# Kernel tuning notes

Measured on AMD Instinct MI355X. Metric: run time of the kernel, lower is better.

The kernel has to match this reference:

```python
import jax, jax.numpy as jnp
import numpy as np

B, N, IN_DIM, D = 32, 2000, 3, 5
GROUP = 5
TOPK = 110

def setup_inputs() -> dict:
    key = jax.random.key(0)
    ks = jax.random.split(key, 11)
    def lin(k, fan_in, fan_out):
        kw, kb = jax.random.split(k)
        bound = 1.0 / np.sqrt(fan_in)
        W = jax.random.uniform(kw, (fan_in, fan_out), jnp.float32, -bound, bound)
        b = jax.random.uniform(kb, (fan_out,), jnp.float32, -bound, bound)
        return W, b
    Wi, bi = lin(ks[1], IN_DIM, D)
    Wq, bq = lin(ks[2], D, D)
    Wk, bk = lin(ks[3], D, D)
    Wv, bv = lin(ks[4], D, D)
    Wo, bo = lin(ks[5], D, D)
    in_mat = jax.random.normal(ks[0], (B, N, IN_DIM), jnp.float32)
    return {"in_mat": in_mat, "Wi": Wi, "bi": bi, "Wq": Wq, "bq": bq,
            "Wk": Wk, "bk": bk, "Wv": Wv, "bv": bv, "Wo": Wo, "bo": bo}

def reference(in_mat, Wi, bi, Wq, bq, Wk, bk, Wv, bv, Wo, bo):
    # input projection: [B,N,3] -> [B,N,D]
    x = in_mat @ Wi + bi
    Q = x @ Wq + bq
    K = x @ Wk + bk
    V = x @ Wv + bv
    scores = jnp.einsum('bnd,bmd->bnm', Q, K) / jnp.sqrt(jnp.float32(D))  # [B,N,N]
    attn = jax.nn.softmax(scores, axis=-1)
    context = jnp.einsum('bnm,bmd->bnd', attn, V)
    _out = context @ Wo + bo  # transformed output (unused downstream, as in source)

    # select_points, fully batched
    diag = jnp.diagonal(attn, axis1=1, axis2=2)               # [B,N]
    attn_sums = diag.reshape(B, N // GROUP, GROUP).sum(-1)    # [B, N/5]
    max_group_idx = jnp.argmax(attn_sums, axis=1)             # [B]
    grp_idx = max_group_idx[:, None] * GROUP + jnp.arange(GROUP)[None, :]  # [B,5]
    group_points = jnp.take_along_axis(in_mat, grp_idx[:, :, None], axis=1)  # [B,5,3]
    centroid = group_points.mean(axis=1)                       # [B,3]
    distances = jnp.linalg.norm(in_mat - centroid[:, None, :], axis=-1)  # [B,N]
    _, closest = jax.lax.top_k(-distances, TOPK)               # smallest distances, [B,110]
    selected = jnp.take_along_axis(in_mat, closest[:, :, None], axis=1)  # [B,110,3]
    return selected
```

## Files before the change

kernel.cpp:

```cpp
#include <hip/hip_runtime.h>
#include <stdint.h>

#define BB     32
#define NN     2000
#define TOPK_  110
#define NBIN   2048

__global__ __launch_bounds__(1024) void k_diag(
    const float* __restrict__ in_mat,
    const float* __restrict__ Wi, const float* __restrict__ bi,
    const float* __restrict__ Wq, const float* __restrict__ bq,
    const float* __restrict__ Wk, const float* __restrict__ bk,
    float* __restrict__ diag_out)
{
    __shared__ float4 Ps[2048];
    __shared__ float  partial[16][256];

    const int b     = blockIdx.y;
    const int chunk = blockIdx.x;
    const int t     = threadIdx.x;
    const float* inb = in_mat + (size_t)b * NN * 3;

    const float pf = 0.44721359549995793f * 1.4426950408889634f;
    float Mq[15], Mk[15], cq[5];
#pragma unroll
    for (int d = 0; d < 5; ++d) {
        float s = bq[d];
#pragma unroll
        for (int k = 0; k < 5; ++k) s += bi[k] * Wq[k * 5 + d];
        cq[d] = s;
    }
#pragma unroll
    for (int i = 0; i < 3; ++i)
#pragma unroll
        for (int d = 0; d < 5; ++d) {
            float sq = 0.f, sk = 0.f;
#pragma unroll
            for (int k = 0; k < 5; ++k) {
                sq += Wi[i * 5 + k] * Wq[k * 5 + d];
                sk += Wi[i * 5 + k] * Wk[k * 5 + d];
            }
            Mq[i * 5 + d] = sq;
            Mk[i * 5 + d] = sk;
        }
    float ck[5];
#pragma unroll
    for (int d = 0; d < 5; ++d) {
        float s = bk[d];
#pragma unroll
        for (int k = 0; k < 5; ++k) s += bi[k] * Wk[k * 5 + d];
        ck[d] = s;
    }
    (void)ck;
    float Gp[3][3], vp[3];
#pragma unroll
    for (int i = 0; i < 3; ++i)
#pragma unroll
        for (int j = 0; j < 3; ++j) {
            float s = 0.f;
#pragma unroll
            for (int d = 0; d < 5; ++d) s += Mq[i * 5 + d] * Mk[j * 5 + d];
            Gp[i][j] = s * pf;
        }
#pragma unroll
    for (int j = 0; j < 3; ++j) {
        float s = 0.f;
#pragma unroll
        for (int d = 0; d < 5; ++d) s += cq[d] * Mk[j * 5 + d];
        vp[j] = s * pf;
    }

#pragma unroll
    for (int r = 0; r < 2; ++r) {
        const int n = r * 1024 + t;
        float4 e = make_float4(0.f, 0.f, 0.f, 0.f);
        if (n < NN) {
            const float p0 = inb[n * 3 + 0];
            const float p1 = inb[n * 3 + 1];
            const float p2 = inb[n * 3 + 2];
            e = make_float4(p0, p1, p2, vp[0] * p0 + vp[1] * p1 + vp[2] * p2);
        }
        Ps[n] = e;
    }

    const int wid  = t >> 6;
    const int lane = t & 63;
    float g[4][3];
#pragma unroll
    for (int r = 0; r < 4; ++r) {
        const int row = chunk * 256 + r * 64 + lane;
        float p0 = 0.f, p1 = 0.f, p2 = 0.f;
        if (row < NN) {
            p0 = inb[row * 3 + 0];
            p1 = inb[row * 3 + 1];
            p2 = inb[row * 3 + 2];
        }
#pragma unroll
        for (int j = 0; j < 3; ++j)
            g[r][j] = p0 * Gp[0][j] + p1 * Gp[1][j] + p2 * Gp[2][j];
    }
    __syncthreads();

    float acc[4] = {0.f, 0.f, 0.f, 0.f};
    const int m0 = wid * (NN / 16);
#pragma unroll 5
    for (int m = m0; m < m0 + NN / 16; ++m) {
        const float4 P = Ps[m];
#pragma unroll
        for (int r = 0; r < 4; ++r) {
            const float e = fmaf(g[r][0], P.x,
                            fmaf(g[r][1], P.y,
                            fmaf(g[r][2], P.z, P.w)));
            acc[r] += __builtin_amdgcn_exp2f(e);
        }
    }
#pragma unroll
    for (int r = 0; r < 4; ++r)
        partial[wid][r * 64 + lane] = acc[r];
    __syncthreads();

    if (t < 256) {
        const int row = chunk * 256 + t;
        if (row < NN) {
            float sum = partial[0][t];
#pragma unroll
            for (int w = 1; w < 16; ++w) sum += partial[w][t];
            const float4 Pr = Ps[row];
            const float gx = Pr.x * Gp[0][0] + Pr.y * Gp[1][0] + Pr.z * Gp[2][0];
            const float gy = Pr.x * Gp[0][1] + Pr.y * Gp[1][1] + Pr.z * Gp[2][1];
            const float gz = Pr.x * Gp[0][2] + Pr.y * Gp[1][2] + Pr.z * Gp[2][2];
            const float e  = fmaf(gx, Pr.x, fmaf(gy, Pr.y, fmaf(gz, Pr.z, Pr.w)));
            diag_out[b * NN + row] = __builtin_amdgcn_exp2f(e) / sum;
        }
    }
}

__global__ __launch_bounds__(1024) void k_select(
    const float* __restrict__ in_mat,
    const float* __restrict__ diag,
    float* __restrict__ out)
{
    __shared__ unsigned long long keys[2048];
    __shared__ unsigned long long cand[2048];
    __shared__ unsigned int       hist[NBIN];
    __shared__ unsigned int       sA[NBIN];
    __shared__ unsigned int       sB[NBIN];
    __shared__ float              wv[16];
    __shared__ int                wi_[16];
    __shared__ float              centroid[3];
    __shared__ int                thrBin, cnt;

    const int b = blockIdx.x;
    const int t = threadIdx.x;
    const float* dg  = diag + (size_t)b * NN;
    const float* inb = in_mat + (size_t)b * NN * 3;

    hist[t] = 0u; hist[t + 1024] = 0u;
    if (t == 0) cnt = 0;

    float v = -INFINITY; int idx = 0x7fffffff;
    if (t < NN / 5) {
        float s = dg[t * 5 + 0];
        s += dg[t * 5 + 1];
        s += dg[t * 5 + 2];
        s += dg[t * 5 + 3];
        s += dg[t * 5 + 4];
        v = s; idx = t;
    }
#pragma unroll
    for (int off = 32; off > 0; off >>= 1) {
        const float ov = __shfl_down(v, off);
        const int   oi = __shfl_down(idx, off);
        if (ov > v || (ov == v && oi < idx)) { v = ov; idx = oi; }
    }
    if ((t & 63) == 0) { wv[t >> 6] = v; wi_[t >> 6] = idx; }
    __syncthreads();
    if (t == 0) {
        float bv = wv[0]; int bidx = wi_[0];
#pragma unroll
        for (int w = 1; w < 16; ++w) {
            if (wv[w] > bv || (wv[w] == bv && wi_[w] < bidx)) {
                bv = wv[w]; bidx = wi_[w];
            }
        }
        const int base = bidx * 5;
#pragma unroll
        for (int d = 0; d < 3; ++d) {
            float s = inb[(base + 0) * 3 + d];
            s = __fadd_rn(s, inb[(base + 1) * 3 + d]);
            s = __fadd_rn(s, inb[(base + 2) * 3 + d]);
            s = __fadd_rn(s, inb[(base + 3) * 3 + d]);
            s = __fadd_rn(s, inb[(base + 4) * 3 + d]);
            centroid[d] = __fdiv_rn(s, 5.0f);
        }
    }
    __syncthreads();

    const float c0 = centroid[0], c1 = centroid[1], c2 = centroid[2];

#pragma unroll
    for (int r = 0; r < 2; ++r) {
        const int n = r * 1024 + t;
        if (n < NN) {
            const float dx = inb[n * 3 + 0] - c0;
            const float dy = inb[n * 3 + 1] - c1;
            const float dz = inb[n * 3 + 2] - c2;
            const float d2 = __fadd_rn(__fadd_rn(__fmul_rn(dx, dx),
                                                 __fmul_rn(dy, dy)),
                                       __fmul_rn(dz, dz));
            const float dist = __fsqrt_rn(d2);
            const unsigned int db = __float_as_uint(dist);
            keys[n] = ((unsigned long long)db << 32) | (unsigned int)n;
            atomicAdd(&hist[db >> 20], 1u);
        }
    }
    __syncthreads();

    unsigned int* src = hist;
    unsigned int* dst = sA;
    for (int stride = 1; stride < NBIN; stride <<= 1) {
#pragma unroll
        for (int r = 0; r < 2; ++r) {
            const int i = r * 1024 + t;
            dst[i] = src[i] + ((i >= stride) ? src[i - stride] : 0u);
        }
        __syncthreads();
        unsigned int* tmp = (dst == sA) ? sB : sA;
        src = dst; dst = (src == hist) ? sA : tmp;
    }
    const unsigned int* cum = src;

#pragma unroll
    for (int r = 0; r < 2; ++r) {
        const int i = r * 1024 + t;
        if (cum[i] >= TOPK_ && (i == 0 || cum[i - 1] < TOPK_)) thrBin = i;
    }
    __syncthreads();

    const int T = thrBin;
#pragma unroll
    for (int r = 0; r < 2; ++r) {
        const int n = r * 1024 + t;
        if (n < NN) {
            const unsigned long long k = keys[n];
            if ((int)(k >> 52) <= T) {
                const int pos = atomicAdd(&cnt, 1);
                cand[pos] = k;
            }
        }
    }
    __syncthreads();

    const int C = cnt;
    for (int i = t; i < C; i += 1024) {
        const unsigned long long ki = cand[i];
        int rank = 0;
        for (int j = 0; j < C; ++j) rank += (cand[j] < ki);
        if (rank < TOPK_) {
            const int n = (int)(unsigned int)(ki & 0xFFFFFFFFull);
            out[((size_t)b * TOPK_ + rank) * 3 + 0] = inb[n * 3 + 0];
            out[((size_t)b * TOPK_ + rank) * 3 + 1] = inb[n * 3 + 1];
            out[((size_t)b * TOPK_ + rank) * 3 + 2] = inb[n * 3 + 2];
        }
    }
}

extern "C" void kernel_launch(void* const* d_in, const int* in_sizes, int n_in,
                              void* d_out, int out_size, void* d_ws, size_t ws_size,
                              hipStream_t stream) {
    const float* in_mat = (const float*)d_in[0];
    const float* Wi = (const float*)d_in[1];
    const float* bi = (const float*)d_in[2];
    const float* Wq = (const float*)d_in[3];
    const float* bq = (const float*)d_in[4];
    const float* Wk = (const float*)d_in[5];
    const float* bk = (const float*)d_in[6];

    float* diag = (float*)d_ws;
    float* out  = (float*)d_out;

    dim3 g1(8, BB);
    k_diag<<<g1, 1024, 0, stream>>>(in_mat, Wi, bi, Wq, bq, Wk, bk, diag);
    k_select<<<BB, 1024, 0, stream>>>(in_mat, diag, out);
}
```

Before: 104.6 us.

## Fuse diagonal and selection kernels using last-block-done atomic counter

Merges the two kernels into one launch: each of the 8 chunk blocks per batch computes its part of the attention diagonal, then increments a per-batch counter, and the last block to finish performs the group argmax, distance histogram and top-k selection. Shared memory for the two phases is overlaid with a union. This removes a kernel launch and the gap between launches, at the cost of a memset launch for the counters and a serialized tail where only 32 blocks do selection work.

```diff
diff --git a/kernel.cpp b/kernel.cpp
--- a/kernel.cpp
+++ b/kernel.cpp
@@ -1,23 +1,45 @@
 #include <hip/hip_runtime.h>
 #include <stdint.h>
 
-#define BB     32
-#define NN     2000
-#define TOPK_  110
-#define NBIN   2048
-
-__global__ __launch_bounds__(1024) void k_diag(
+#define BB      32
+#define NN      2000
+#define TOPK_   110
+#define NBIN    2048
+#define CHUNKS  8
+#define ROWS    256
+
+union SMem {
+    struct {
+        float4 Ps[2048];
+        float  partial[16][256];
+    } a;
+    struct {
+        unsigned long long keys[2048];
+        unsigned long long cand[2048];
+        unsigned int       hist[NBIN];
+        unsigned int       sA[NBIN];
+        unsigned int       sB[NBIN];
+    } b;
+};
+
+__global__ __launch_bounds__(1024) void k_fused(
     const float* __restrict__ in_mat,
     const float* __restrict__ Wi, const float* __restrict__ bi,
     const float* __restrict__ Wq, const float* __restrict__ bq,
     const float* __restrict__ Wk, const float* __restrict__ bk,
-    float* __restrict__ diag_out)
+    float* __restrict__ diag,
+    unsigned int* __restrict__ counters,
+    float* __restrict__ out)
 {
-    __shared__ float4 Ps[2048];
-    __shared__ float  partial[16][256];
-
-    const int b     = blockIdx.y;
-    const int chunk = blockIdx.x;
+    __shared__ SMem  sm;
+    __shared__ float wv[16];
+    __shared__ int   wi_[16];
+    __shared__ float centroid[3];
+    __shared__ int   thrBin, cnt, isLast;
+
+    const int bid   = blockIdx.x;
+    const int b     = bid >> 3;
+    const int chunk = bid & (CHUNKS - 1);
     const int t     = threadIdx.x;
     const float* inb = in_mat + (size_t)b * NN * 3;
 
@@ -43,15 +65,6 @@
             Mq[i * 5 + d] = sq;
             Mk[i * 5 + d] = sk;
         }
-    float ck[5];
-#pragma unroll
-    for (int d = 0; d < 5; ++d) {
-        float s = bk[d];
-#pragma unroll
-        for (int k = 0; k < 5; ++k) s += bi[k] * Wk[k * 5 + d];
-        ck[d] = s;
-    }
-    (void)ck;
     float Gp[3][3], vp[3];
 #pragma unroll
     for (int i = 0; i < 3; ++i)
@@ -80,7 +93,7 @@
             const float p2 = inb[n * 3 + 2];
             e = make_float4(p0, p1, p2, vp[0] * p0 + vp[1] * p1 + vp[2] * p2);
         }
-        Ps[n] = e;
+        sm.a.Ps[n] = e;
     }
 
     const int wid  = t >> 6;
@@ -88,7 +101,7 @@
     float g[4][3];
 #pragma unroll
     for (int r = 0; r < 4; ++r) {
-        const int row = chunk * 256 + r * 64 + lane;
+        const int row = chunk * ROWS + r * 64 + lane;
         float p0 = 0.f, p1 = 0.f, p2 = 0.f;
         if (row < NN) {
             p0 = inb[row * 3 + 0];
@@ -105,7 +118,7 @@
     const int m0 = wid * (NN / 16);
 #pragma unroll 5
     for (int m = m0; m < m0 + NN / 16; ++m) {
-        const float4 P = Ps[m];
+        const float4 P = sm.a.Ps[m];
 #pragma unroll
         for (int r = 0; r < 4; ++r) {
             const float e = fmaf(g[r][0], P.x,
@@ -116,48 +129,38 @@
     }
 #pragma unroll
     for (int r = 0; r < 4; ++r)
-        partial[wid][r * 64 + lane] = acc[r];
-    __syncthreads();
-
-    if (t < 256) {
-        const int row = chunk * 256 + t;
+        sm.a.partial[wid][r * 64 + lane] = acc[r];
+    __syncthreads();
+
+    if (t < ROWS) {
+        const int row = chunk * ROWS + t;
         if (row < NN) {
-            float sum = partial[0][t];
-#pragma unroll
-            for (int w = 1; w < 16; ++w) sum += partial[w][t];
-            const float4 Pr = Ps[row];
+            float sum = sm.a.partial[0][t];
+#pragma unroll
+            for (int w = 1; w < 16; ++w) sum += sm.a.partial[w][t];
+            const float4 Pr = sm.a.Ps[row];
             const float gx = Pr.x * Gp[0][0] + Pr.y * Gp[1][0] + Pr.z * Gp[2][0];
             const float gy = Pr.x * Gp[0][1] + Pr.y * Gp[1][1] + Pr.z * Gp[2][1];
             const float gz = Pr.x * Gp[0][2] + Pr.y * Gp[1][2] + Pr.z * Gp[2][2];
             const float e  = fmaf(gx, Pr.x, fmaf(gy, Pr.y, fmaf(gz, Pr.z, Pr.w)));
-            diag_out[b * NN + row] = __builtin_amdgcn_exp2f(e) / sum;
-        }
-    }
-}
-
-__global__ __launch_bounds__(1024) void k_select(
-    const float* __restrict__ in_mat,
-    const float* __restrict__ diag,
-    float* __restrict__ out)
-{
-    __shared__ unsigned long long keys[2048];
-    __shared__ unsigned long long cand[2048];
-    __shared__ unsigned int       hist[NBIN];
-    __shared__ unsigned int       sA[NBIN];
-    __shared__ unsigned int       sB[NBIN];
-    __shared__ float              wv[16];
-    __shared__ int                wi_[16];
-    __shared__ float              centroid[3];
-    __shared__ int                thrBin, cnt;
-
-    const int b = blockIdx.x;
-    const int t = threadIdx.x;
-    const float* dg  = diag + (size_t)b * NN;
-    const float* inb = in_mat + (size_t)b * NN * 3;
-
-    hist[t] = 0u; hist[t + 1024] = 0u;
-    if (t == 0) cnt = 0;
-
+            diag[b * NN + row] = __builtin_amdgcn_exp2f(e) / sum;
+        }
+    }
+    __syncthreads();
+
+    if (t == 0) {
+        __threadfence();
+        const unsigned old = atomicAdd(&counters[b], 1u);
+        isLast = (old == CHUNKS - 1) ? 1 : 0;
+        cnt = 0;
+    }
+    __syncthreads();
+    if (!isLast) return;
+    __threadfence();
+
+    const float* dg = diag + (size_t)b * NN;
+
+    sm.b.hist[t] = 0u; sm.b.hist[t + 1024] = 0u;
     float v = -INFINITY; int idx = 0x7fffffff;
     if (t < NN / 5) {
         float s = dg[t * 5 + 0];
@@ -175,6 +178,7 @@
     }
     if ((t & 63) == 0) { wv[t >> 6] = v; wi_[t >> 6] = idx; }
     __syncthreads();
+
     if (t == 0) {
         float bv = wv[0]; int bidx = wi_[0];
 #pragma unroll
@@ -210,14 +214,14 @@
                                        __fmul_rn(dz, dz));
             const float dist = __fsqrt_rn(d2);
             const unsigned int db = __float_as_uint(dist);
-            keys[n] = ((unsigned long long)db << 32) | (unsigned int)n;
-            atomicAdd(&hist[db >> 20], 1u);
-        }
-    }
-    __syncthreads();
-
-    unsigned int* src = hist;
-    unsigned int* dst = sA;
+            sm.b.keys[n] = ((unsigned long long)db << 32) | (unsigned int)n;
+            atomicAdd(&sm.b.hist[db >> 20], 1u);
+        }
+    }
+    __syncthreads();
+
+    unsigned int* src = sm.b.hist;
+    unsigned int* dst = sm.b.sA;
     for (int stride = 1; stride < NBIN; stride <<= 1) {
 #pragma unroll
         for (int r = 0; r < 2; ++r) {
@@ -225,8 +229,8 @@
             dst[i] = src[i] + ((i >= stride) ? src[i - stride] : 0u);
         }
         __syncthreads();
-        unsigned int* tmp = (dst == sA) ? sB : sA;
-        src = dst; dst = (src == hist) ? sA : tmp;
+        unsigned int* tmp = (dst == sm.b.sA) ? sm.b.sB : sm.b.sA;
+        src = dst; dst = (src == sm.b.hist) ? sm.b.sA : tmp;
     }
     const unsigned int* cum = src;
 
@@ -242,10 +246,10 @@
     for (int r = 0; r < 2; ++r) {
         const int n = r * 1024 + t;
         if (n < NN) {
-            const unsigned long long k = keys[n];
+            const unsigned long long k = sm.b.keys[n];
             if ((int)(k >> 52) <= T) {
                 const int pos = atomicAdd(&cnt, 1);
-                cand[pos] = k;
+                sm.b.cand[pos] = k;
             }
         }
     }
@@ -253,9 +257,9 @@
 
     const int C = cnt;
     for (int i = t; i < C; i += 1024) {
-        const unsigned long long ki = cand[i];
+        const unsigned long long ki = sm.b.cand[i];
         int rank = 0;
-        for (int j = 0; j < C; ++j) rank += (cand[j] < ki);
+        for (int j = 0; j < C; ++j) rank += (sm.b.cand[j] < ki);
         if (rank < TOPK_) {
             const int n = (int)(unsigned int)(ki & 0xFFFFFFFFull);
             out[((size_t)b * TOPK_ + rank) * 3 + 0] = inb[n * 3 + 0];
@@ -276,10 +280,11 @@
     const float* Wk = (const float*)d_in[5];
     const float* bk = (const float*)d_in[6];
 
-    float* diag = (float*)d_ws;
-    float* out  = (float*)d_out;
-
-    dim3 g1(8, BB);
-    k_diag<<<g1, 1024, 0, stream>>>(in_mat, Wi, bi, Wq, bq, Wk, bk, diag);
-    k_select<<<BB, 1024, 0, stream>>>(in_mat, diag, out);
+    float*        diag     = (float*)d_ws;
+    unsigned int* counters = (unsigned int*)((char*)d_ws + 256 * 1024);
+    float*        out      = (float*)d_out;
+
+    hipMemsetAsync(counters, 0, BB * sizeof(unsigned int), stream);
+    k_fused<<<dim3(BB * CHUNKS), 1024, 0, stream>>>(
+        in_mat, Wi, bi, Wq, bq, Wk, bk, diag, counters, out);
 }
```

Result: slower. 135.7 us (+29.8%).

## Split diag column range across two blocks with atomic row sums, finish in select

Applied to the files above, without the earlier changes.

The softmax-denominator computation now splits the column (m) range into two halves, doubling the grid to 16x32 blocks. Each block atomically adds its partial row sums into a zeroed workspace. The diagonal numerator and the division are moved into k_select, which refolds the weights and computes the diagonal in shared memory. This is meant to raise occupancy and parallelism on the dominant O(N^2) kernel, at the cost of an extra memset launch, float atomics (order-dependent rounding), and extra per-point work in the select kernel.

```diff
diff --git a/kernel.cpp b/kernel.cpp
--- a/kernel.cpp
+++ b/kernel.cpp
@@ -1,26 +1,17 @@
 #include <hip/hip_runtime.h>
 #include <stdint.h>
 
-#define BB     32
-#define NN     2000
-#define TOPK_  110
-#define NBIN   2048
-
-__global__ __launch_bounds__(1024) void k_diag(
-    const float* __restrict__ in_mat,
+#define BB      32
+#define NN      2000
+#define TOPK_   110
+#define NBIN    2048
+
+__device__ __forceinline__ void fold_weights(
     const float* __restrict__ Wi, const float* __restrict__ bi,
     const float* __restrict__ Wq, const float* __restrict__ bq,
     const float* __restrict__ Wk, const float* __restrict__ bk,
-    float* __restrict__ diag_out)
+    float Gp[3][3], float vp[3])
 {
-    __shared__ float4 Ps[2048];
-    __shared__ float  partial[16][256];
-
-    const int b     = blockIdx.y;
-    const int chunk = blockIdx.x;
-    const int t     = threadIdx.x;
-    const float* inb = in_mat + (size_t)b * NN * 3;
-
     const float pf = 0.44721359549995793f * 1.4426950408889634f;
     float Mq[15], Mk[15], cq[5];
 #pragma unroll
@@ -43,16 +34,6 @@
             Mq[i * 5 + d] = sq;
             Mk[i * 5 + d] = sk;
         }
-    float ck[5];
-#pragma unroll
-    for (int d = 0; d < 5; ++d) {
-        float s = bk[d];
-#pragma unroll
-        for (int k = 0; k < 5; ++k) s += bi[k] * Wk[k * 5 + d];
-        ck[d] = s;
-    }
-    (void)ck;
-    float Gp[3][3], vp[3];
 #pragma unroll
     for (int i = 0; i < 3; ++i)
 #pragma unroll
@@ -69,18 +50,34 @@
         for (int d = 0; d < 5; ++d) s += cq[d] * Mk[j * 5 + d];
         vp[j] = s * pf;
     }
-
-#pragma unroll
-    for (int r = 0; r < 2; ++r) {
-        const int n = r * 1024 + t;
-        float4 e = make_float4(0.f, 0.f, 0.f, 0.f);
-        if (n < NN) {
-            const float p0 = inb[n * 3 + 0];
-            const float p1 = inb[n * 3 + 1];
-            const float p2 = inb[n * 3 + 2];
-            e = make_float4(p0, p1, p2, vp[0] * p0 + vp[1] * p1 + vp[2] * p2);
-        }
-        Ps[n] = e;
+}
+
+__global__ __launch_bounds__(1024) void k_diag(
+    const float* __restrict__ in_mat,
+    const float* __restrict__ Wi, const float* __restrict__ bi,
+    const float* __restrict__ Wq, const float* __restrict__ bq,
+    const float* __restrict__ Wk, const float* __restrict__ bk,
+    float* __restrict__ sums)
+{
+    __shared__ float4 Ps[1024];
+    __shared__ float  partial[16][256];
+
+    const int b   = blockIdx.y;
+    const int rc  = blockIdx.x >> 1;
+    const int ms  = blockIdx.x & 1;
+    const int t   = threadIdx.x;
+    const float* inb = in_mat + (size_t)b * NN * 3;
+
+    float Gp[3][3], vp[3];
+    fold_weights(Wi, bi, Wq, bq, Wk, bk, Gp, vp);
+
+    if (t < 1000) {
+        const int n = ms * 1000 + t;
+        const float p0 = inb[n * 3 + 0];
+        const float p1 = inb[n * 3 + 1];
+        const float p2 = inb[n * 3 + 2];
+        Ps[t] = make_float4(p0, p1, p2,
+                            vp[0] * p0 + vp[1] * p1 + vp[2] * p2);
     }
 
     const int wid  = t >> 6;
@@ -88,7 +85,7 @@
     float g[4][3];
 #pragma unroll
     for (int r = 0; r < 4; ++r) {
-        const int row = chunk * 256 + r * 64 + lane;
+        const int row = rc * 256 + r * 64 + lane;
         float p0 = 0.f, p1 = 0.f, p2 = 0.f;
         if (row < NN) {
             p0 = inb[row * 3 + 0];
@@ -101,10 +98,10 @@
     }
     __syncthreads();
 
+    const int start = wid * 62 + (wid < 8 ? wid : 8);
+    const int len   = 62 + (wid < 8 ? 1 : 0);
     float acc[4] = {0.f, 0.f, 0.f, 0.f};
-    const int m0 = wid * (NN / 16);
-#pragma unroll 5
-    for (int m = m0; m < m0 + NN / 16; ++m) {
+    for (int m = start; m < start + len; ++m) {
         const float4 P = Ps[m];
 #pragma unroll
         for (int r = 0; r < 4; ++r) {
@@ -120,51 +117,71 @@
     __syncthreads();
 
     if (t < 256) {
-        const int row = chunk * 256 + t;
+        const int row = rc * 256 + t;
         if (row < NN) {
-            float sum = partial[0][t];
-#pragma unroll
-            for (int w = 1; w < 16; ++w) sum += partial[w][t];
-            const float4 Pr = Ps[row];
-            const float gx = Pr.x * Gp[0][0] + Pr.y * Gp[1][0] + Pr.z * Gp[2][0];
-            const float gy = Pr.x * Gp[0][1] + Pr.y * Gp[1][1] + Pr.z * Gp[2][1];
-            const float gz = Pr.x * Gp[0][2] + Pr.y * Gp[1][2] + Pr.z * Gp[2][2];
-            const float e  = fmaf(gx, Pr.x, fmaf(gy, Pr.y, fmaf(gz, Pr.z, Pr.w)));
-            diag_out[b * NN + row] = __builtin_amdgcn_exp2f(e) / sum;
+            float s = partial[0][t];
+#pragma unroll
+            for (int w = 1; w < 16; ++w) s += partial[w][t];
+            atomicAdd(&sums[(size_t)b * NN + row], s);
         }
     }
 }
 
 __global__ __launch_bounds__(1024) void k_select(
     const float* __restrict__ in_mat,
-    const float* __restrict__ diag,
+    const float* __restrict__ sums,
+    const float* __restrict__ Wi, const float* __restrict__ bi,
+    const float* __restrict__ Wq, const float* __restrict__ bq,
+    const float* __restrict__ Wk, const float* __restrict__ bk,
     float* __restrict__ out)
 {
     __shared__ unsigned long long keys[2048];
-    __shared__ unsigned long long cand[2048];
-    __shared__ unsigned int       hist[NBIN];
-    __shared__ unsigned int       sA[NBIN];
-    __shared__ unsigned int       sB[NBIN];
-    __shared__ float              wv[16];
-    __shared__ int                wi_[16];
-    __shared__ float              centroid[3];
-    __shared__ int                thrBin, cnt;
+    __shared__ union {
+        float              dg[2048];
+        unsigned long long cand[2048];
+    } u;
+    __shared__ unsigned int hist[NBIN];
+    __shared__ unsigned int sA[NBIN];
+    __shared__ unsigned int sB[NBIN];
+    __shared__ float        wv[16];
+    __shared__ int          wi_[16];
+    __shared__ float        centroid[3];
+    __shared__ int          thrBin, cnt;
 
     const int b = blockIdx.x;
     const int t = threadIdx.x;
-    const float* dg  = diag + (size_t)b * NN;
+    const float* sb  = sums + (size_t)b * NN;
     const float* inb = in_mat + (size_t)b * NN * 3;
+
+    float Gp[3][3], vp[3];
+    fold_weights(Wi, bi, Wq, bq, Wk, bk, Gp, vp);
 
     hist[t] = 0u; hist[t + 1024] = 0u;
     if (t == 0) cnt = 0;
+#pragma unroll
+    for (int r = 0; r < 2; ++r) {
+        const int n = r * 1024 + t;
+        if (n < NN) {
+            const float p0 = inb[n * 3 + 0];
+            const float p1 = inb[n * 3 + 1];
+            const float p2 = inb[n * 3 + 2];
+            const float gx = p0 * Gp[0][0] + p1 * Gp[1][0] + p2 * Gp[2][0];
+            const float gy = p0 * Gp[0][1] + p1 * Gp[1][1] + p2 * Gp[2][1];
+            const float gz = p0 * Gp[0][2] + p1 * Gp[1][2] + p2 * Gp[2][2];
+            const float bw = vp[0] * p0 + vp[1] * p1 + vp[2] * p2;
+            const float e  = fmaf(gx, p0, fmaf(gy, p1, fmaf(gz, p2, bw)));
+            u.dg[n] = __builtin_amdgcn_exp2f(e) / sb[n];
+        }
+    }
+    __syncthreads();
 
     float v = -INFINITY; int idx = 0x7fffffff;
     if (t < NN / 5) {
-        float s = dg[t * 5 + 0];
-        s += dg[t * 5 + 1];
-        s += dg[t * 5 + 2];
-        s += dg[t * 5 + 3];
-        s += dg[t * 5 + 4];
+        float s = u.dg[t * 5 + 0];
+        s += u.dg[t * 5 + 1];
+        s += u.dg[t * 5 + 2];
+        s += u.dg[t * 5 + 3];
+        s += u.dg[t * 5 + 4];
         v = s; idx = t;
     }
 #pragma unroll
@@ -175,6 +192,7 @@
     }
     if ((t & 63) == 0) { wv[t >> 6] = v; wi_[t >> 6] = idx; }
     __syncthreads();
+
     if (t == 0) {
         float bv = wv[0]; int bidx = wi_[0];
 #pragma unroll
@@ -245,7 +263,7 @@
             const unsigned long long k = keys[n];
             if ((int)(k >> 52) <= T) {
                 const int pos = atomicAdd(&cnt, 1);
-                cand[pos] = k;
+                u.cand[pos] = k;
             }
         }
     }
@@ -253,9 +271,9 @@
 
     const int C = cnt;
     for (int i = t; i < C; i += 1024) {
-        const unsigned long long ki = cand[i];
+        const unsigned long long ki = u.cand[i];
         int rank = 0;
-        for (int j = 0; j < C; ++j) rank += (cand[j] < ki);
+        for (int j = 0; j < C; ++j) rank += (u.cand[j] < ki);
         if (rank < TOPK_) {
             const int n = (int)(unsigned int)(ki & 0xFFFFFFFFull);
             out[((size_t)b * TOPK_ + rank) * 3 + 0] = inb[n * 3 + 0];
@@ -276,10 +294,12 @@
     const float* Wk = (const float*)d_in[5];
     const float* bk = (const float*)d_in[6];
 
-    float* diag = (float*)d_ws;
+    float* sums = (float*)d_ws;
     float* out  = (float*)d_out;
 
-    dim3 g1(8, BB);
-    k_diag<<<g1, 1024, 0, stream>>>(in_mat, Wi, bi, Wq, bq, Wk, bk, diag);
-    k_select<<<BB, 1024, 0, stream>>>(in_mat, diag, out);
+    hipMemsetAsync(sums, 0, (size_t)BB * NN * sizeof(float), stream);
+    k_diag<<<dim3(16, BB), 1024, 0, stream>>>(
+        in_mat, Wi, bi, Wq, bq, Wk, bk, sums);
+    k_select<<<BB, 1024, 0, stream>>>(
+        in_mat, sums, Wi, bi, Wq, bq, Wk, bk, out);
 }
```

After: 109.5 us. +4.7%, slower.

## Split diag rows across more blocks and stream key points from global memory

Applied to the files above, without the earlier changes.

The diagonal-softmax kernel now gives each block 128 rows instead of 256, doubling the grid to 16x32 blocks. It no longer stages all points into shared memory as float4. Each wave reads its 125 key points straight from global memory, which drops a sync and the staging pass. The bias term vp is folded into the per-row coefficients, so each score uses three FMAs with no precomputed w term. The trade is fewer rows per thread to reuse each point load (2 instead of 4), repeated global or cache reads of in_mat, and duplicated weight folding across more blocks.

```diff
diff --git a/kernel.cpp b/kernel.cpp
--- a/kernel.cpp
+++ b/kernel.cpp
@@ -1,26 +1,17 @@
 #include <hip/hip_runtime.h>
 #include <stdint.h>
 
-#define BB     32
-#define NN     2000
-#define TOPK_  110
-#define NBIN   2048
-
-__global__ __launch_bounds__(1024) void k_diag(
-    const float* __restrict__ in_mat,
+#define BB      32
+#define NN      2000
+#define TOPK_   110
+#define NBIN    2048
+
+__device__ __forceinline__ void fold_weights(
     const float* __restrict__ Wi, const float* __restrict__ bi,
     const float* __restrict__ Wq, const float* __restrict__ bq,
     const float* __restrict__ Wk, const float* __restrict__ bk,
-    float* __restrict__ diag_out)
+    float Gp[3][3], float vp[3])
 {
-    __shared__ float4 Ps[2048];
-    __shared__ float  partial[16][256];
-
-    const int b     = blockIdx.y;
-    const int chunk = blockIdx.x;
-    const int t     = threadIdx.x;
-    const float* inb = in_mat + (size_t)b * NN * 3;
-
     const float pf = 0.44721359549995793f * 1.4426950408889634f;
     float Mq[15], Mk[15], cq[5];
 #pragma unroll
@@ -43,16 +34,6 @@
             Mq[i * 5 + d] = sq;
             Mk[i * 5 + d] = sk;
         }
-    float ck[5];
-#pragma unroll
-    for (int d = 0; d < 5; ++d) {
-        float s = bk[d];
-#pragma unroll
-        for (int k = 0; k < 5; ++k) s += bi[k] * Wk[k * 5 + d];
-        ck[d] = s;
-    }
-    (void)ck;
-    float Gp[3][3], vp[3];
 #pragma unroll
     for (int i = 0; i < 3; ++i)
 #pragma unroll
@@ -69,26 +50,31 @@
         for (int d = 0; d < 5; ++d) s += cq[d] * Mk[j * 5 + d];
         vp[j] = s * pf;
     }
-
-#pragma unroll
-    for (int r = 0; r < 2; ++r) {
-        const int n = r * 1024 + t;
-        float4 e = make_float4(0.f, 0.f, 0.f, 0.f);
-        if (n < NN) {
-            const float p0 = inb[n * 3 + 0];
-            const float p1 = inb[n * 3 + 1];
-            const float p2 = inb[n * 3 + 2];
-            e = make_float4(p0, p1, p2, vp[0] * p0 + vp[1] * p1 + vp[2] * p2);
-        }
-        Ps[n] = e;
-    }
-
-    const int wid  = t >> 6;
+}
+
+__global__ __launch_bounds__(1024) void k_diag(
+    const float* __restrict__ in_mat,
+    const float* __restrict__ Wi, const float* __restrict__ bi,
+    const float* __restrict__ Wq, const float* __restrict__ bq,
+    const float* __restrict__ Wk, const float* __restrict__ bk,
+    float* __restrict__ diag)
+{
+    __shared__ float partial[16][128];
+
+    const int b   = blockIdx.y;
+    const int rc  = blockIdx.x;
+    const int t   = threadIdx.x;
+    const int wid = t >> 6;
     const int lane = t & 63;
-    float g[4][3];
-#pragma unroll
-    for (int r = 0; r < 4; ++r) {
-        const int row = chunk * 256 + r * 64 + lane;
+    const float* inb = in_mat + (size_t)b * NN * 3;
+
+    float Gp[3][3], vp[3];
+    fold_weights(Wi, bi, Wq, bq, Wk, bk, Gp, vp);
+
+    float h[2][3];
+#pragma unroll
+    for (int r = 0; r < 2; ++r) {
+        const int row = rc * 128 + r * 64 + lane;
         float p0 = 0.f, p1 = 0.f, p2 = 0.f;
         if (row < NN) {
             p0 = inb[row * 3 + 0];
@@ -97,40 +83,40 @@
         }
 #pragma unroll
         for (int j = 0; j < 3; ++j)
-            g[r][j] = p0 * Gp[0][j] + p1 * Gp[1][j] + p2 * Gp[2][j];
-    }
-    __syncthreads();
-
-    float acc[4] = {0.f, 0.f, 0.f, 0.f};
-    const int m0 = wid * (NN / 16);
+            h[r][j] = p0 * Gp[0][j] + p1 * Gp[1][j] + p2 * Gp[2][j] + vp[j];
+    }
+
+    float acc0 = 0.f, acc1 = 0.f;
+    const int m0 = wid * 125;
 #pragma unroll 5
-    for (int m = m0; m < m0 + NN / 16; ++m) {
-        const float4 P = Ps[m];
-#pragma unroll
-        for (int r = 0; r < 4; ++r) {
-            const float e = fmaf(g[r][0], P.x,
-                            fmaf(g[r][1], P.y,
-                            fmaf(g[r][2], P.z, P.w)));
-            acc[r] += __builtin_amdgcn_exp2f(e);
-        }
-    }
-#pragma unroll
-    for (int r = 0; r < 4; ++r)
-        partial[wid][r * 64 + lane] = acc[r];
-    __syncthreads();
-
-    if (t < 256) {
-        const int row = chunk * 256 + t;
+    for (int m = m0; m < m0 + 125; ++m) {
+        const float px = inb[m * 3 + 0];
+        const float py = inb[m * 3 + 1];
+        const float pz = inb[m * 3 + 2];
+        const float e0 = fmaf(h[0][0], px, fmaf(h[0][1], py, h[0][2] * pz));
+        const float e1 = fmaf(h[1][0], px, fmaf(h[1][1], py, h[1][2] * pz));
+        acc0 += __builtin_amdgcn_exp2f(e0);
+        acc1 += __builtin_amdgcn_exp2f(e1);
+    }
+    partial[wid][lane]      = acc0;
+    partial[wid][64 + lane] = acc1;
+    __syncthreads();
+
+    if (t < 128) {
+        const int row = rc * 128 + t;
         if (row < NN) {
             float sum = partial[0][t];
 #pragma unroll
             for (int w = 1; w < 16; ++w) sum += partial[w][t];
-            const float4 Pr = Ps[row];
-            const float gx = Pr.x * Gp[0][0] + Pr.y * Gp[1][0] + Pr.z * Gp[2][0];
-            const float gy = Pr.x * Gp[0][1] + Pr.y * Gp[1][1] + Pr.z * Gp[2][1];
-            const float gz = Pr.x * Gp[0][2] + Pr.y * Gp[1][2] + Pr.z * Gp[2][2];
-            const float e  = fmaf(gx, Pr.x, fmaf(gy, Pr.y, fmaf(gz, Pr.z, Pr.w)));
-            diag_out[b * NN + row] = __builtin_amdgcn_exp2f(e) / sum;
+            const float p0 = inb[row * 3 + 0];
+            const float p1 = inb[row * 3 + 1];
+            const float p2 = inb[row * 3 + 2];
+            float hh[3];
+#pragma unroll
+            for (int j = 0; j < 3; ++j)
+                hh[j] = p0 * Gp[0][j] + p1 * Gp[1][j] + p2 * Gp[2][j] + vp[j];
+            const float e = fmaf(hh[0], p0, fmaf(hh[1], p1, hh[2] * p2));
+            diag[(size_t)b * NN + row] = __builtin_amdgcn_exp2f(e) / sum;
         }
     }
 }
@@ -142,13 +128,13 @@
 {
     __shared__ unsigned long long keys[2048];
     __shared__ unsigned long long cand[2048];
-    __shared__ unsigned int       hist[NBIN];
-    __shared__ unsigned int       sA[NBIN];
-    __shared__ unsigned int       sB[NBIN];
-    __shared__ float              wv[16];
-    __shared__ int                wi_[16];
-    __shared__ float              centroid[3];
-    __shared__ int                thrBin, cnt;
+    __shared__ unsigned int hist[NBIN];
+    __shared__ unsigned int sA[NBIN];
+    __shared__ unsigned int sB[NBIN];
+    __shared__ float        wv[16];
+    __shared__ int          wi_[16];
+    __shared__ float        centroid[3];
+    __shared__ int          thrBin, cnt;
 
     const int b = blockIdx.x;
     const int t = threadIdx.x;
@@ -175,6 +161,7 @@
     }
     if ((t & 63) == 0) { wv[t >> 6] = v; wi_[t >> 6] = idx; }
     __syncthreads();
+
     if (t == 0) {
         float bv = wv[0]; int bidx = wi_[0];
 #pragma unroll
@@ -279,7 +266,7 @@
     float* diag = (float*)d_ws;
     float* out  = (float*)d_out;
 
-    dim3 g1(8, BB);
-    k_diag<<<g1, 1024, 0, stream>>>(in_mat, Wi, bi, Wq, bq, Wk, bk, diag);
+    k_diag<<<dim3(16, BB), 1024, 0, stream>>>(
+        in_mat, Wi, bi, Wq, bq, Wk, bk, diag);
     k_select<<<BB, 1024, 0, stream>>>(in_mat, diag, out);
 }
```

Measured after the change: 113.0 us. 8.1% more time.
